# Optimization experiments

Measured on AMD Instinct MI355X. Metric: run time of the kernel, lower is better.

## Reference

```python
import jax, jax.numpy as jnp
import numpy as np
import math

B, S, H, D = 2, 2048, 12, 768


def setup_inputs() -> dict:
    key = jax.random.key(0)
    ks = jax.random.split(key, 7)
    std = 0.02
    x = jax.random.normal(ks[0], (B, S, D), jnp.float32)
    W_q = std * jax.random.normal(ks[1], (H, D, D), jnp.float32)
    W_k = std * jax.random.normal(ks[2], (H, D, D), jnp.float32)
    W_v = std * jax.random.normal(ks[3], (H, D, D), jnp.float32)
    W_o = (std / math.sqrt(2 * 12)) * jax.random.normal(ks[4], (D, H * D), jnp.float32)
    ff_w1 = std * jax.random.normal(ks[5], (4 * D, D), jnp.float32)
    ff_w2 = std * jax.random.normal(ks[6], (D, 4 * D), jnp.float32)
    return {"x": x, "W_q": W_q, "W_k": W_k, "W_v": W_v, "W_o": W_o,
            "ff_w1": ff_w1, "ff_w2": ff_w2}


def _layernorm(x, eps=1e-5):
    # LayerNorm(elementwise_affine=False)
    mu = jnp.mean(x, axis=-1, keepdims=True)
    var = jnp.var(x, axis=-1, keepdims=True)
    return (x - mu) * jax.lax.rsqrt(var + eps)


def reference(x, W_q, W_k, W_v, W_o, ff_w1, ff_w2):
    b, s, d = x.shape
    h = W_q.shape[0]
    # per-head FULL-width projections: x is shared across heads
    Q = jnp.einsum('bsd,hde->bhse', x, W_q)
    K = jnp.einsum('bsd,hde->bhse', x, W_k)
    V = jnp.einsum('bsd,hde->bhse', x, W_v)
    scores = jnp.einsum('bhqe,bhke->bhqk', Q, K) / math.sqrt(d)  # [B,H,S,S]
    causal = jnp.tril(jnp.ones((s, s), dtype=bool))
    scores = jnp.where(causal[None, None], scores, jnp.finfo(scores.dtype).min)
    attn = jax.nn.softmax(scores, axis=-1)
    ctx = jnp.einsum('bhqk,bhke->bhqe', attn, V)            # [B,H,S,D]
    ctx = ctx.transpose(0, 2, 1, 3).reshape(b, s, h * d)     # [B,S,H*D]
    out = ctx @ W_o.T                                        # [B,S,D]
    # FFN: LN(no affine) -> Linear(d,4d) -> GELU(exact) -> Linear(4d,d); dropout=eval no-op
    hdn = jax.nn.gelu(_layernorm(out) @ ff_w1.T, approximate=False)
    out = out + hdn @ ff_w2.T
    return out
```

## Files before the change

kernel.cpp:

```cpp
#include <hip/hip_runtime.h>
#include <math.h>

#define S_   2048
#define D_   768
#define HD_  9216
#define FF_  3072

typedef float  f32x4  __attribute__((ext_vector_type(4)));
typedef __bf16 bf16x8 __attribute__((ext_vector_type(8)));

__device__ __forceinline__ ushort f2bf(float v) {
    return __builtin_bit_cast(ushort, (__bf16)v);
}

__device__ __forceinline__ void load_lds16(const ushort* g, ushort* l) {
    __builtin_amdgcn_global_load_lds(
        (const __attribute__((address_space(1))) void*)g,
        (__attribute__((address_space(3))) void*)l, 16, 0, 0);
}

__device__ __forceinline__ void zero_acc(f32x4 acc[4][4]) {
#pragma unroll
    for (int i = 0; i < 4; ++i)
#pragma unroll
        for (int j = 0; j < 4; ++j) acc[i][j] = (f32x4){0.f, 0.f, 0.f, 0.f};
}

__device__ __forceinline__ void gemm128(
    const ushort* __restrict__ A, int lda,
    const ushort* __restrict__ Bt, int ldb,
    int m0, int n0, int kmax, f32x4 acc[4][4])
{
    __shared__ __align__(16) ushort As[2][128 * 32];
    __shared__ __align__(16) ushort Bs[2][128 * 32];
    const int tid  = threadIdx.x;
    const int lane = tid & 63, wave = tid >> 6;
    const int l16  = lane & 15, quad = lane >> 4;
    const int wr = wave >> 1, wc = wave & 1;
    const int srow = lane >> 2;
    const int scol = (lane & 3) << 3;

    const ushort* Ab = A + (size_t)m0 * lda;
    const ushort* Bb = Bt + (size_t)n0 * ldb;

    auto stage = [&](int k0, int buf) {
#pragma unroll
        for (int c = 0; c < 2; ++c) {
            const int rb = c * 64 + wave * 16;
            load_lds16(Ab + (size_t)(rb + srow) * lda + k0 + scol,
                       &As[buf][rb * 32]);
            load_lds16(Bb + (size_t)(rb + srow) * ldb + k0 + scol,
                       &Bs[buf][rb * 32]);
        }
    };

    stage(0, 0);
    __syncthreads();
    int cur = 0;
    for (int k0 = 0; k0 < kmax; k0 += 32) {
        if (k0 + 32 < kmax) stage(k0 + 32, cur ^ 1);
        bf16x8 a[4], b[4];
#pragma unroll
        for (int i = 0; i < 4; ++i)
            a[i] = *(const bf16x8*)&As[cur][(wr * 64 + i * 16 + l16) * 32 + quad * 8];
#pragma unroll
        for (int j = 0; j < 4; ++j)
            b[j] = *(const bf16x8*)&Bs[cur][(wc * 64 + j * 16 + l16) * 32 + quad * 8];
#pragma unroll
        for (int i = 0; i < 4; ++i)
#pragma unroll
            for (int j = 0; j < 4; ++j)
                acc[i][j] = __builtin_amdgcn_mfma_f32_16x16x32_bf16(
                    a[i], b[j], acc[i][j], 0, 0, 0);
        __syncthreads();
        cur ^= 1;
    }
}

__device__ __forceinline__ void gemm128_bA(
    const ushort* __restrict__ Ab,
    const ushort* __restrict__ Bt, int ldb,
    int n0, int kmax, f32x4 acc[4][4])
{
    __shared__ __align__(16) ushort As[2][128 * 32];
    __shared__ __align__(16) ushort Bs[2][128 * 32];
    const int tid  = threadIdx.x;
    const int lane = tid & 63, wave = tid >> 6;
    const int l16  = lane & 15, quad = lane >> 4;
    const int wr = wave >> 1, wc = wave & 1;
    const int srow = lane >> 2;
    const int scol = (lane & 3) << 3;

    const ushort* Bb = Bt + (size_t)n0 * ldb;

    auto stage = [&](int k0, int buf) {
        const ushort* At = Ab + (size_t)(k0 >> 7) * 16384 + (k0 & 127);
#pragma unroll
        for (int c = 0; c < 2; ++c) {
            const int rb = c * 64 + wave * 16;
            load_lds16(At + (size_t)(rb + srow) * 128 + scol, &As[buf][rb * 32]);
            load_lds16(Bb + (size_t)(rb + srow) * ldb + k0 + scol,
                       &Bs[buf][rb * 32]);
        }
    };

    stage(0, 0);
    __syncthreads();
    int cur = 0;
    for (int k0 = 0; k0 < kmax; k0 += 32) {
        if (k0 + 32 < kmax) stage(k0 + 32, cur ^ 1);
        bf16x8 a[4], b[4];
#pragma unroll
        for (int i = 0; i < 4; ++i)
            a[i] = *(const bf16x8*)&As[cur][(wr * 64 + i * 16 + l16) * 32 + quad * 8];
#pragma unroll
        for (int j = 0; j < 4; ++j)
            b[j] = *(const bf16x8*)&Bs[cur][(wc * 64 + j * 16 + l16) * 32 + quad * 8];
#pragma unroll
        for (int i = 0; i < 4; ++i)
#pragma unroll
            for (int j = 0; j < 4; ++j)
                acc[i][j] = __builtin_amdgcn_mfma_f32_16x16x32_bf16(
                    a[i], b[j], acc[i][j], 0, 0, 0);
        __syncthreads();
        cur ^= 1;
    }
}

#define EPI_DECL \
    const int lane_ = threadIdx.x & 63, wave_ = threadIdx.x >> 6;   \
    const int l16_ = lane_ & 15, quad_ = lane_ >> 4;                \
    const int wr_ = wave_ >> 1, wc_ = wave_ & 1;
#define RR_ (wr_ * 64 + i * 16 + quad_ * 4 + r)
#define NC_ (wc_ * 64 + j * 16 + l16_)

__global__ __launch_bounds__(256) void convert_kernel(
    const float* __restrict__ in, ushort* __restrict__ out, long n)
{
    long i = ((long)blockIdx.x * 256 + threadIdx.x) * 4;
    const long stride = (long)gridDim.x * 1024;
    for (; i < n; i += stride) {
        float4 v = *(const float4*)&in[i];
        out[i + 0] = f2bf(v.x); out[i + 1] = f2bf(v.y);
        out[i + 2] = f2bf(v.z); out[i + 3] = f2bf(v.w);
    }
}

__global__ __launch_bounds__(256, 2) void gemmNT_kernel(
    const ushort* __restrict__ A, int lda, long aStr,
    const ushort* __restrict__ Bt, int ldb, long bStr,
    ushort* __restrict__ C, int ldc, long cStr, int kmax)
{
    const int z = blockIdx.z;
    const int m0 = blockIdx.y * 128, n0 = blockIdx.x * 128;
    f32x4 acc[4][4];
    zero_acc(acc);
    gemm128(A + (size_t)z * aStr, lda, Bt + (size_t)z * bStr, ldb,
            m0, n0, kmax, acc);
    ushort* out = C + (size_t)z * cStr;
    EPI_DECL
#pragma unroll
    for (int i = 0; i < 4; ++i)
#pragma unroll
        for (int j = 0; j < 4; ++j)
#pragma unroll
            for (int r = 0; r < 4; ++r)
                out[(size_t)(m0 + RR_) * ldc + n0 + NC_] = f2bf(acc[i][j][r]);
}

__global__ __launch_bounds__(256, 2) void xmy_kernel(
    const ushort* __restrict__ Xb, const ushort* __restrict__ MtP,
    const ushort* __restrict__ UtP, ushort* __restrict__ XMp,
    ushort* __restrict__ Yt)
{
    const int z = blockIdx.z;
    const int h = z & 1;
    const bool ymode = z >= 2;
    const int m0 = blockIdx.y * 128, n0 = blockIdx.x * 128;
    const ushort* Bt = (ymode ? UtP : MtP) + (size_t)h * 589824;
    f32x4 acc[4][4];
    zero_acc(acc);
    gemm128(Xb, D_, Bt, D_, m0, n0, D_, acc);
    EPI_DECL
    if (!ymode) {
        ushort* out = XMp + (size_t)h * 3145728;
#pragma unroll
        for (int i = 0; i < 4; ++i)
#pragma unroll
            for (int j = 0; j < 4; ++j)
#pragma unroll
                for (int r = 0; r < 4; ++r)
                    out[(size_t)(m0 + RR_) * D_ + n0 + NC_] = f2bf(acc[i][j][r]);
    } else {
        const int b = m0 >> 11;
        ushort* out = Yt + (size_t)h * 3145728 + (size_t)b * 1572864;
#pragma unroll
        for (int i = 0; i < 4; ++i)
#pragma unroll
            for (int j = 0; j < 4; ++j) {
                ushort4 o4;
                o4.x = f2bf(acc[i][j][0]); o4.y = f2bf(acc[i][j][1]);
                o4.z = f2bf(acc[i][j][2]); o4.w = f2bf(acc[i][j][3]);
                const int nc = n0 + wc_ * 64 + j * 16 + l16_;
                const int s  = (m0 & 2047) + wr_ * 64 + i * 16 + quad_ * 4;
                *(ushort4*)&out[(size_t)nc * 2048 + s] = o4;
            }
    }
}

__global__ __launch_bounds__(256, 2) void scores_c_kernel(
    const ushort* __restrict__ XM, const ushort* __restrict__ Xb,
    ushort* __restrict__ Sc)
{
    const int t = blockIdx.x, b = blockIdx.y, hp = blockIdx.z;
    int mi = (int)((sqrtf(8.f * t + 1.f) - 1.f) * 0.5f);
    while ((mi + 1) * (mi + 2) / 2 <= t) ++mi;
    while (mi * (mi + 1) / 2 > t) --mi;
    const int ni = t - mi * (mi + 1) / 2;
    f32x4 acc[4][4];
    zero_acc(acc);
    gemm128(XM + (size_t)hp * 3145728 + (size_t)b * 1572864, D_,
            Xb + (size_t)b * 1572864, D_, mi * 128, ni * 128, D_, acc);
    ushort* out = Sc + ((size_t)(hp * 2 + b) * 136 + t) * 16384;
    EPI_DECL
#pragma unroll
    for (int i = 0; i < 4; ++i)
#pragma unroll
        for (int j = 0; j < 4; ++j)
#pragma unroll
            for (int r = 0; r < 4; ++r)
                out[(size_t)RR_ * 128 + NC_] = f2bf(acc[i][j][r]);
}

__global__ __launch_bounds__(256) void softmax_c_kernel(ushort* __restrict__ Sc)
{
    const int bx = blockIdx.x;
    const int hp = bx >> 12, b = (bx >> 11) & 1, q = bx & 2047;
    ushort* base = Sc + (size_t)((hp * 2 + b) * 136) * 16384;
    const int mi = q >> 7, tri = mi * (mi + 1) / 2;
    const int L  = (mi + 1) << 7;
    const int ro = (q & 127) << 7;
    const float scale = 0.03608439182435161f;
    const int tid = threadIdx.x;
    const int wave = tid >> 6, lane = tid & 63;

    float xv[8];
    float m = -1e30f;
#pragma unroll
    for (int i = 0; i < 2; ++i) {
        const int k = tid * 4 + i * 1024;
        ushort4 v = {0, 0, 0, 0};
        if (k <= q)
            v = *(const ushort4*)&base[(size_t)(tri + (k >> 7)) * 16384
                                       + ro + (k & 127)];
        xv[i * 4 + 0] = (k + 0 <= q) ? (float)*(__bf16*)&v.x * scale : -1e30f;
        xv[i * 4 + 1] = (k + 1 <= q) ? (float)*(__bf16*)&v.y * scale : -1e30f;
        xv[i * 4 + 2] = (k + 2 <= q) ? (float)*(__bf16*)&v.z * scale : -1e30f;
        xv[i * 4 + 3] = (k + 3 <= q) ? (float)*(__bf16*)&v.w * scale : -1e30f;
#pragma unroll
        for (int j = 0; j < 4; ++j) m = fmaxf(m, xv[i * 4 + j]);
    }
    for (int o = 32; o > 0; o >>= 1) m = fmaxf(m, __shfl_xor(m, o));
    __shared__ float redm[4];
    if (lane == 0) redm[wave] = m;
    __syncthreads();
    m = fmaxf(fmaxf(redm[0], redm[1]), fmaxf(redm[2], redm[3]));

    float e[8];
    float s = 0.f;
#pragma unroll
    for (int i = 0; i < 2; ++i) {
        const int k = tid * 4 + i * 1024;
#pragma unroll
        for (int j = 0; j < 4; ++j) {
            e[i * 4 + j] = (k + j <= q) ? __expf(xv[i * 4 + j] - m) : 0.f;
            s += e[i * 4 + j];
        }
    }
    for (int o = 32; o > 0; o >>= 1) s += __shfl_xor(s, o);
    __shared__ float reds[4];
    if (lane == 0) reds[wave] = s;
    __syncthreads();
    s = reds[0] + reds[1] + reds[2] + reds[3];
    const float inv = 1.f / s;
#pragma unroll
    for (int i = 0; i < 2; ++i) {
        const int k = tid * 4 + i * 1024;
        if (k < L) {
            ushort4 o4;
            o4.x = f2bf(e[i * 4 + 0] * inv);
            o4.y = f2bf(e[i * 4 + 1] * inv);
            o4.z = f2bf(e[i * 4 + 2] * inv);
            o4.w = f2bf(e[i * 4 + 3] * inv);
            *(ushort4*)&base[(size_t)(tri + (k >> 7)) * 16384
                             + ro + (k & 127)] = o4;
        }
    }
}

__global__ __launch_bounds__(256, 2) void py_kernel(
    const ushort* __restrict__ Sc, const ushort* __restrict__ Yt,
    float* __restrict__ Attn)
{
    const int z = blockIdx.z;
    const int h = z & 1, b = (z >> 1) & 1, kh = z >> 2;
    const int mi = 15 - blockIdx.y;
    const int n0 = blockIdx.x * 128;
    const int ktiles = mi + 1;
    const int split  = (ktiles + 1) >> 1;
    const int t0 = kh ? split : 0;
    const int t1 = kh ? ktiles : split;
    if (t0 >= t1) return;
    const ushort* Ab =
        Sc + ((size_t)(h * 2 + b) * 136 + mi * (mi + 1) / 2 + t0) * 16384;
    const ushort* Bt = Yt + (size_t)h * 3145728 + (size_t)b * 1572864
                     + (size_t)t0 * 128;
    f32x4 acc[4][4];
    zero_acc(acc);
    gemm128_bA(Ab, Bt, S_, n0, (t1 - t0) * 128, acc);
    float* out = Attn + (size_t)b * 1572864 + (size_t)mi * 128 * D_;
    EPI_DECL
#pragma unroll
    for (int i = 0; i < 4; ++i)
#pragma unroll
        for (int j = 0; j < 4; ++j)
#pragma unroll
            for (int r = 0; r < 4; ++r)
                unsafeAtomicAdd(&out[(size_t)RR_ * D_ + n0 + NC_],
                                acc[i][j][r]);
}

__global__ __launch_bounds__(256) void ln_kernel(
    const float* __restrict__ Attn, ushort* __restrict__ Ln)
{
    const int row = blockIdx.x;
    const float* a = Attn + (size_t)row * D_;
    const int tid = threadIdx.x;
    const int wave = tid >> 6, lane = tid & 63;
    float v0 = a[tid], v1 = a[tid + 256], v2 = a[tid + 512];
    float s  = v0 + v1 + v2;
    float sq = v0 * v0 + v1 * v1 + v2 * v2;
    for (int o = 32; o > 0; o >>= 1) { s += __shfl_xor(s, o); sq += __shfl_xor(sq, o); }
    __shared__ float rs[4], rq[4];
    if (lane == 0) { rs[wave] = s; rq[wave] = sq; }
    __syncthreads();
    s  = rs[0] + rs[1] + rs[2] + rs[3];
    sq = rq[0] + rq[1] + rq[2] + rq[3];
    const float mean = s * (1.f / 768.f);
    float var = sq * (1.f / 768.f) - mean * mean;
    var = fmaxf(var, 0.f);
    const float rstd = rsqrtf(var + 1e-5f);
    ushort* o = Ln + (size_t)row * D_;
    o[tid]       = f2bf((v0 - mean) * rstd);
    o[tid + 256] = f2bf((v1 - mean) * rstd);
    o[tid + 512] = f2bf((v2 - mean) * rstd);
}

__global__ __launch_bounds__(256, 2) void ffn1_kernel(
    const ushort* __restrict__ Ln, const ushort* __restrict__ F1b,
    ushort* __restrict__ H1)
{
    const int m0 = blockIdx.y * 128, n0 = blockIdx.x * 128;
    f32x4 acc[4][4];
    zero_acc(acc);
    gemm128(Ln, D_, F1b, D_, m0, n0, D_, acc);
    EPI_DECL
#pragma unroll
    for (int i = 0; i < 4; ++i)
#pragma unroll
        for (int j = 0; j < 4; ++j)
#pragma unroll
            for (int r = 0; r < 4; ++r) {
                float v = acc[i][j][r];
                float gl = 0.5f * v * (1.f + erff(v * 0.70710678118654752f));
                H1[(size_t)(m0 + RR_) * FF_ + n0 + NC_] = f2bf(gl);
            }
}

__global__ __launch_bounds__(256) void copyres_kernel(
    const float* __restrict__ Attn, float* __restrict__ Out)
{
    const long i = ((long)blockIdx.x * 256 + threadIdx.x) * 4;
    *(float4*)&Out[i] = *(const float4*)&Attn[i];
}

__global__ __launch_bounds__(256, 2) void ffn2a_kernel(
    const ushort* __restrict__ H1, const ushort* __restrict__ F2b,
    float* __restrict__ Out)
{
    const int z = blockIdx.z;
    const int m0 = blockIdx.y * 128, n0 = blockIdx.x * 128;
    f32x4 acc[4][4];
    zero_acc(acc);
    gemm128(H1 + (size_t)z * 768, FF_, F2b + (size_t)z * 768, FF_,
            m0, n0, 768, acc);
    EPI_DECL
#pragma unroll
    for (int i = 0; i < 4; ++i)
#pragma unroll
        for (int j = 0; j < 4; ++j)
#pragma unroll
            for (int r = 0; r < 4; ++r)
                unsafeAtomicAdd(&Out[(size_t)(m0 + RR_) * D_ + n0 + NC_],
                                acc[i][j][r]);
}

extern "C" void kernel_launch(void* const* d_in, const int* in_sizes, int n_in,
                              void* d_out, int out_size, void* d_ws, size_t ws_size,
                              hipStream_t stream)
{
    int ix = -1, iw[4], nw = 0, iff[2], nf = 0;
    for (int i = 0; i < 7; ++i) {
        long sz = in_sizes[i];
        if (sz == 3145728L) ix = i;
        else if (sz == 2359296L) { if (nf < 2) iff[nf++] = i; }
        else { if (nw < 4) iw[nw++] = i; }
    }
    if (ix < 0 || nw != 4 || nf != 2) {
        ix = 0; iw[0] = 1; iw[1] = 2; iw[2] = 3; iw[3] = 4; iff[0] = 5; iff[1] = 6;
    }
    const float* x; const float *Wq, *Wk, *Wv, *Wo, *F1, *F2;
    x  = (const float*)d_in[ix];
    F1 = (const float*)d_in[iff[0]];
    F2 = (const float*)d_in[iff[1]];
    if (ix == 0) {
        Wq = (const float*)d_in[iw[0]]; Wk = (const float*)d_in[iw[1]];
        Wv = (const float*)d_in[iw[2]]; Wo = (const float*)d_in[iw[3]];
    } else {
        Wk = (const float*)d_in[iw[0]]; Wo = (const float*)d_in[iw[1]];
        Wq = (const float*)d_in[iw[2]]; Wv = (const float*)d_in[iw[3]];
    }

    char* p = (char*)d_ws;
    ushort* Xb   = (ushort*)(p + 0);
    ushort* Mt   = (ushort*)(p + 6291456);
    ushort* Ut   = (ushort*)(p + 20447232);
    float*  Attn = (float*) (p + 34603008);
    ushort* XMp  = (ushort*)(p + 47185920);
    ushort* Yt   = (ushort*)(p + 59768832);
    ushort* Scp  = (ushort*)(p + 72351744);
    ushort* Wa   = (ushort*)(p + 47185920);
    ushort* Wb   = (ushort*)(p + 61341696);
    ushort* H1   = (ushort*)(p + 0);
    ushort* F1b  = (ushort*)(p + 47185920);
    ushort* F2b  = (ushort*)(p + 51904512);
    ushort* Ln   = (ushort*)(p + 56623104);

    dim3 blk(256);
    hipMemsetAsync(Attn, 0, 12582912, stream);

    convert_kernel<<<dim3(1024), blk, 0, stream>>>(x, Xb, 3145728L);

    convert_kernel<<<dim3(1024), blk, 0, stream>>>(Wq, Wa, 7077888L);
    convert_kernel<<<dim3(1024), blk, 0, stream>>>(Wk, Wb, 7077888L);
    gemmNT_kernel<<<dim3(6, 6, 12), blk, 0, stream>>>(
        Wb, 768, 589824L, Wa, 768, 589824L, Mt, 768, 589824L, 768);
    convert_kernel<<<dim3(1024), blk, 0, stream>>>(Wv, Wa, 7077888L);
    convert_kernel<<<dim3(1024), blk, 0, stream>>>(Wo, Wb, 7077888L);
    gemmNT_kernel<<<dim3(6, 6, 12), blk, 0, stream>>>(
        Wb, HD_, 768L, Wa, 768, 589824L, Ut, 768, 589824L, 768);

    for (int pr = 0; pr < 6; ++pr) {
        xmy_kernel<<<dim3(6, 32, 4), blk, 0, stream>>>(
            Xb, Mt + (size_t)pr * 1179648, Ut + (size_t)pr * 1179648,
            XMp, Yt);
        scores_c_kernel<<<dim3(136, 2, 2), blk, 0, stream>>>(XMp, Xb, Scp);
        softmax_c_kernel<<<dim3(8192), blk, 0, stream>>>(Scp);
        py_kernel<<<dim3(6, 16, 8), blk, 0, stream>>>(Scp, Yt, Attn);
    }

    convert_kernel<<<dim3(1024), blk, 0, stream>>>(F1, F1b, 2359296L);
    convert_kernel<<<dim3(1024), blk, 0, stream>>>(F2, F2b, 2359296L);
    ln_kernel<<<dim3(4096), blk, 0, stream>>>(Attn, Ln);
    copyres_kernel<<<dim3(3072), blk, 0, stream>>>(Attn, (float*)d_out);
    ffn1_kernel<<<dim3(24, 32), blk, 0, stream>>>(Ln, F1b, H1);
    ffn2a_kernel<<<dim3(6, 32, 4), blk, 0, stream>>>(H1, F2b, (float*)d_out);
}
```

Measured before the change: 1.068 ms.

## Replace atomic accumulation with per-head buffers and deterministic split-K reduction

The attention-output kernel drops its K-split and atomic adds. Each of the two heads in a pair now writes into its own fp32 accumulator, one in workspace and one in the output buffer, using plain read-modify-write. The FFN second GEMM becomes a 2-way split writing partials, and a final elementwise kernel sums the partials, both attention buffers and the residual. This removes the atomic contention and the residual copy kernel, at the cost of fewer py blocks (less parallelism on short causal rows) and an extra reduction pass.

```diff
diff --git a/kernel.cpp b/kernel.cpp
--- a/kernel.cpp
+++ b/kernel.cpp
@@ -300,25 +300,20 @@
 
 __global__ __launch_bounds__(256, 2) void py_kernel(
     const ushort* __restrict__ Sc, const ushort* __restrict__ Yt,
-    float* __restrict__ Attn)
+    float* __restrict__ AttnA, float* __restrict__ AttnB)
 {
     const int z = blockIdx.z;
-    const int h = z & 1, b = (z >> 1) & 1, kh = z >> 2;
+    const int h = z >> 1, b = z & 1;
     const int mi = 15 - blockIdx.y;
     const int n0 = blockIdx.x * 128;
-    const int ktiles = mi + 1;
-    const int split  = (ktiles + 1) >> 1;
-    const int t0 = kh ? split : 0;
-    const int t1 = kh ? ktiles : split;
-    if (t0 >= t1) return;
     const ushort* Ab =
-        Sc + ((size_t)(h * 2 + b) * 136 + mi * (mi + 1) / 2 + t0) * 16384;
-    const ushort* Bt = Yt + (size_t)h * 3145728 + (size_t)b * 1572864
-                     + (size_t)t0 * 128;
-    f32x4 acc[4][4];
-    zero_acc(acc);
-    gemm128_bA(Ab, Bt, S_, n0, (t1 - t0) * 128, acc);
-    float* out = Attn + (size_t)b * 1572864 + (size_t)mi * 128 * D_;
+        Sc + ((size_t)(h * 2 + b) * 136 + mi * (mi + 1) / 2) * 16384;
+    const ushort* Bt = Yt + (size_t)h * 3145728 + (size_t)b * 1572864;
+    f32x4 acc[4][4];
+    zero_acc(acc);
+    gemm128_bA(Ab, Bt, S_, n0, (mi + 1) << 7, acc);
+    float* out = (h ? AttnB : AttnA) + (size_t)b * 1572864
+               + (size_t)mi * 128 * D_;
     EPI_DECL
 #pragma unroll
     for (int i = 0; i < 4; ++i)
@@ -326,18 +321,21 @@
         for (int j = 0; j < 4; ++j)
 #pragma unroll
             for (int r = 0; r < 4; ++r)
-                unsafeAtomicAdd(&out[(size_t)RR_ * D_ + n0 + NC_],
-                                acc[i][j][r]);
+                out[(size_t)RR_ * D_ + n0 + NC_] += acc[i][j][r];
 }
 
 __global__ __launch_bounds__(256) void ln_kernel(
-    const float* __restrict__ Attn, ushort* __restrict__ Ln)
+    const float* __restrict__ AttnA, const float* __restrict__ AttnB,
+    ushort* __restrict__ Ln)
 {
     const int row = blockIdx.x;
-    const float* a = Attn + (size_t)row * D_;
+    const float* a = AttnA + (size_t)row * D_;
+    const float* b = AttnB + (size_t)row * D_;
     const int tid = threadIdx.x;
     const int wave = tid >> 6, lane = tid & 63;
-    float v0 = a[tid], v1 = a[tid + 256], v2 = a[tid + 512];
+    float v0 = a[tid]       + b[tid];
+    float v1 = a[tid + 256] + b[tid + 256];
+    float v2 = a[tid + 512] + b[tid + 512];
     float s  = v0 + v1 + v2;
     float sq = v0 * v0 + v1 * v1 + v2 * v2;
     for (int o = 32; o > 0; o >>= 1) { s += __shfl_xor(s, o); sq += __shfl_xor(sq, o); }
@@ -377,23 +375,17 @@
             }
 }
 
-__global__ __launch_bounds__(256) void copyres_kernel(
-    const float* __restrict__ Attn, float* __restrict__ Out)
-{
-    const long i = ((long)blockIdx.x * 256 + threadIdx.x) * 4;
-    *(float4*)&Out[i] = *(const float4*)&Attn[i];
-}
-
-__global__ __launch_bounds__(256, 2) void ffn2a_kernel(
+__global__ __launch_bounds__(256, 2) void ffn2p_kernel(
     const ushort* __restrict__ H1, const ushort* __restrict__ F2b,
-    float* __restrict__ Out)
+    float* __restrict__ P2)
 {
     const int z = blockIdx.z;
     const int m0 = blockIdx.y * 128, n0 = blockIdx.x * 128;
     f32x4 acc[4][4];
     zero_acc(acc);
-    gemm128(H1 + (size_t)z * 768, FF_, F2b + (size_t)z * 768, FF_,
-            m0, n0, 768, acc);
+    gemm128(H1 + (size_t)z * 1536, FF_, F2b + (size_t)z * 1536, FF_,
+            m0, n0, 1536, acc);
+    float* out = P2 + (size_t)z * 3145728;
     EPI_DECL
 #pragma unroll
     for (int i = 0; i < 4; ++i)
@@ -401,8 +393,22 @@
         for (int j = 0; j < 4; ++j)
 #pragma unroll
             for (int r = 0; r < 4; ++r)
-                unsafeAtomicAdd(&Out[(size_t)(m0 + RR_) * D_ + n0 + NC_],
-                                acc[i][j][r]);
+                out[(size_t)(m0 + RR_) * D_ + n0 + NC_] = acc[i][j][r];
+}
+
+__global__ __launch_bounds__(256) void ffn2r_kernel(
+    const float* __restrict__ P2, const float* __restrict__ AttnA,
+    float* __restrict__ Out)
+{
+    const long i = ((long)blockIdx.x * 256 + threadIdx.x) * 4;
+    float4 a = *(const float4*)&P2[i];
+    float4 b = *(const float4*)&P2[3145728 + i];
+    float4 c = *(const float4*)&AttnA[i];
+    float4 d = *(const float4*)&Out[i];
+    float4 o;
+    o.x = a.x + b.x + c.x + d.x; o.y = a.y + b.y + c.y + d.y;
+    o.z = a.z + b.z + c.z + d.z; o.w = a.w + b.w + c.w + d.w;
+    *(float4*)&Out[i] = o;
 }
 
 extern "C" void kernel_launch(void* const* d_in, const int* in_sizes, int n_in,
@@ -432,22 +438,25 @@
     }
 
     char* p = (char*)d_ws;
-    ushort* Xb   = (ushort*)(p + 0);
-    ushort* Mt   = (ushort*)(p + 6291456);
-    ushort* Ut   = (ushort*)(p + 20447232);
-    float*  Attn = (float*) (p + 34603008);
-    ushort* XMp  = (ushort*)(p + 47185920);
-    ushort* Yt   = (ushort*)(p + 59768832);
-    ushort* Scp  = (ushort*)(p + 72351744);
-    ushort* Wa   = (ushort*)(p + 47185920);
-    ushort* Wb   = (ushort*)(p + 61341696);
-    ushort* H1   = (ushort*)(p + 0);
-    ushort* F1b  = (ushort*)(p + 47185920);
-    ushort* F2b  = (ushort*)(p + 51904512);
-    ushort* Ln   = (ushort*)(p + 56623104);
+    ushort* Xb    = (ushort*)(p + 0);
+    ushort* Mt    = (ushort*)(p + 6291456);
+    ushort* Ut    = (ushort*)(p + 20447232);
+    float*  AttnA = (float*) (p + 34603008);
+    ushort* XMp   = (ushort*)(p + 47185920);
+    ushort* Yt    = (ushort*)(p + 59768832);
+    ushort* Scp   = (ushort*)(p + 72351744);
+    float*  AttnB = (float*)d_out;
+    ushort* Wa    = (ushort*)(p + 47185920);
+    ushort* Wb    = (ushort*)(p + 61341696);
+    ushort* H1    = (ushort*)(p + 0);
+    ushort* F1b   = (ushort*)(p + 47185920);
+    ushort* F2b   = (ushort*)(p + 51904512);
+    ushort* Ln    = (ushort*)(p + 56623104);
+    float*  P2    = (float*) (p + 62914560);
 
     dim3 blk(256);
-    hipMemsetAsync(Attn, 0, 12582912, stream);
+    hipMemsetAsync(AttnA, 0, 12582912, stream);
+    hipMemsetAsync(AttnB, 0, 12582912, stream);
 
     convert_kernel<<<dim3(1024), blk, 0, stream>>>(x, Xb, 3145728L);
 
@@ -466,13 +475,13 @@
             XMp, Yt);
         scores_c_kernel<<<dim3(136, 2, 2), blk, 0, stream>>>(XMp, Xb, Scp);
         softmax_c_kernel<<<dim3(8192), blk, 0, stream>>>(Scp);
-        py_kernel<<<dim3(6, 16, 8), blk, 0, stream>>>(Scp, Yt, Attn);
+        py_kernel<<<dim3(6, 16, 4), blk, 0, stream>>>(Scp, Yt, AttnA, AttnB);
     }
 
     convert_kernel<<<dim3(1024), blk, 0, stream>>>(F1, F1b, 2359296L);
     convert_kernel<<<dim3(1024), blk, 0, stream>>>(F2, F2b, 2359296L);
-    ln_kernel<<<dim3(4096), blk, 0, stream>>>(Attn, Ln);
-    copyres_kernel<<<dim3(3072), blk, 0, stream>>>(Attn, (float*)d_out);
+    ln_kernel<<<dim3(4096), blk, 0, stream>>>(AttnA, AttnB, Ln);
     ffn1_kernel<<<dim3(24, 32), blk, 0, stream>>>(Ln, F1b, H1);
-    ffn2a_kernel<<<dim3(6, 32, 4), blk, 0, stream>>>(H1, F2b, (float*)d_out);
-}
+    ffn2p_kernel<<<dim3(6, 32, 2), blk, 0, stream>>>(H1, F2b, P2);
+    ffn2r_kernel<<<dim3(3072), blk, 0, stream>>>(P2, AttnA, (float*)d_out);
+}
```

Result: faster. 1.028 ms (-3.8%).
